# Kernel tuning notes

Measured on AMD Instinct MI355X. Metric: run time of the kernel, lower is better.

## Reference

```python
import jax, jax.numpy as jnp
import numpy as np

B, T, F, K = 32, 1500, 512, 31
QBITS = 8
EPS = 1e-5


def fake_quant(x, bits=QBITS):
    """Symmetric per-tensor fake quantization (scale from dynamic max-abs),
    with straight-through estimator so gradients pass through unchanged."""
    qmax = 2.0 ** (bits - 1) - 1.0  # 127 for 8 bits
    scale = jnp.maximum(jnp.max(jnp.abs(x)) / qmax, 1e-8)
    q = jnp.clip(jnp.round(x / scale), -qmax - 1.0, qmax) * scale
    return x + jax.lax.stop_gradient(q - x)


def setup_inputs() -> dict:
    key = jax.random.key(0)
    ks = jax.random.split(key, 5)
    x = jax.random.normal(ks[0], (B, T, F), dtype=jnp.float32)
    W1 = jax.random.normal(ks[1], (2 * F, F), dtype=jnp.float32) * (1.0 / np.sqrt(F))
    b1 = jnp.zeros((2 * F,), jnp.float32)
    dw_w = jax.random.normal(ks[2], (F, 1, K), dtype=jnp.float32) * (1.0 / np.sqrt(K))
    dw_b = jnp.zeros((F,), jnp.float32)
    W2 = jax.random.normal(ks[3], (F, F), dtype=jnp.float32) * (1.0 / np.sqrt(F))
    b2 = jnp.zeros((F,), jnp.float32)
    return {
        "x": x,
        "ln_gamma": jnp.ones((F,), jnp.float32),
        "ln_beta": jnp.zeros((F,), jnp.float32),
        "W1": W1, "b1": b1,
        "dw_w": dw_w, "dw_b": dw_b,
        "bn_gamma": jnp.ones((F,), jnp.float32),
        "bn_beta": jnp.zeros((F,), jnp.float32),
        "W2": W2, "b2": b2,
    }


def _forward(x, ln_gamma, ln_beta, W1, b1, dw_w, dw_b, bn_gamma, bn_beta, W2, b2):
    # LayerNorm over last dim F
    mu = jnp.mean(x, axis=-1, keepdims=True)
    var = jnp.mean(jnp.square(x - mu), axis=-1, keepdims=True)
    t = (x - mu) * jax.lax.rsqrt(var + EPS) * ln_gamma + ln_beta

    # pconv1 in-quant -> quantized pointwise conv1 (Linear F -> 2F) -> out-quant
    t = fake_quant(t)
    t = jnp.einsum("btf,gf->btg", t, fake_quant(W1)) + b1
    t = fake_quant(t)

    # GLU over last dim: [B,T,2F] -> [B,T,F]
    a, g = jnp.split(t, 2, axis=-1)
    t = a * jax.nn.sigmoid(g)

    # depthwise conv on [B,F,T]
    t = jnp.transpose(t, (0, 2, 1))  # [B,F,T]
    t = fake_quant(t)
    t = jax.lax.conv_general_dilated(
        t, fake_quant(dw_w),
        window_strides=(1,),
        padding=[((K - 1) // 2, (K - 1) // 2)],
        feature_group_count=F,
        dimension_numbers=("NCH", "OIH", "NCH"),
    ) + dw_b[None, :, None]
    t = fake_quant(t)

    # BatchNorm1d over channel dim (stats over batch and time), training-style batch stats
    bmu = jnp.mean(t, axis=(0, 2), keepdims=True)
    bvar = jnp.mean(jnp.square(t - bmu), axis=(0, 2), keepdims=True)
    t = (t - bmu) * jax.lax.rsqrt(bvar + EPS) * bn_gamma[None, :, None] + bn_beta[None, :, None]

    t = jnp.transpose(t, (0, 2, 1))  # [B,T,F]
    t = jax.nn.silu(t)

    # pconv2 in-quant -> quantized pointwise conv2 (Linear F -> F) -> out-quant
    t = fake_quant(t)
    t = jnp.einsum("btf,gf->btg", t, fake_quant(W2)) + b2
    t = fake_quant(t)
    return t  # dropout is identity (p=0 / eval)


def reference(x, ln_gamma, ln_beta, W1, b1, dw_w, dw_b, bn_gamma, bn_beta, W2, b2):
    return _forward(x, ln_gamma, ln_beta, W1, b1, dw_w, dw_b, bn_gamma, bn_beta, W2, b2)
```

## Files before the change

kernel.cpp:

```cpp
#include <hip/hip_runtime.h>
#include <stdint.h>

typedef __bf16 bf16;
typedef __bf16   bf16x4 __attribute__((ext_vector_type(4)));
typedef __bf16   bf16x8 __attribute__((ext_vector_type(8)));
typedef short    s16x8  __attribute__((ext_vector_type(8)));
typedef float    fx4    __attribute__((ext_vector_type(4)));

#define NB 32
#define NT 1500
#define NF 512
#define NM (NB*NT)
#define KW 31
#define EPSF 1e-5f

__device__ __forceinline__ float dscale(const float* a) {
  return fmaxf(a[0] * (1.0f/127.0f), 1e-8f);
}
__device__ __forceinline__ float fq_int(float x, float inv_s) {
  return fminf(fmaxf(rintf(x*inv_s), -128.0f), 127.0f);
}
__device__ __forceinline__ void block_amax(float v, float* dst) {
  __shared__ float red[8];
  #pragma unroll
  for (int o = 32; o > 0; o >>= 1) v = fmaxf(v, __shfl_xor(v, o));
  if ((threadIdx.x & 63) == 0) red[threadIdx.x >> 6] = v;
  __syncthreads();
  if (threadIdx.x == 0) {
    int nw = blockDim.x >> 6;
    float m = red[0];
    for (int i = 1; i < nw; i++) m = fmaxf(m, red[i]);
    atomicMax((unsigned int*)dst, __float_as_uint(m));
  }
}

__device__ __forceinline__ float amax_loop(const float* p, long n4, int bid, int gsz) {
  float am = 0.f;
  long i = (long)bid * blockDim.x + threadIdx.x;
  long stride = (long)gsz * blockDim.x;
  for (; i < n4; i += stride) {
    fx4 v = ((const fx4*)p)[i];
    #pragma unroll
    for (int j = 0; j < 4; j++) am = fmaxf(am, fabsf(v[j]));
  }
  return am;
}
__global__ void absmax_w(const float* __restrict__ W1, const float* __restrict__ W2,
                         const float* __restrict__ dwp, float* a) {
  int bx = blockIdx.x;
  float am; float* dst;
  if (bx < 256)      { am = amax_loop(W1,  131072, bx,       256); dst = a + 1; }
  else if (bx < 384) { am = amax_loop(W2,  65536,  bx - 256, 128); dst = a + 2; }
  else               { am = amax_loop(dwp, 3968,   bx - 384, 8);   dst = a + 3; }
  block_amax(am, dst);
}

__global__ void quant_pack(const float* __restrict__ src, bf16* __restrict__ dst,
                           int R, const float* amax) {
  float inv_s = 1.0f / dscale(amax);
  int total = R * 64;
  for (int t = blockIdx.x*blockDim.x + threadIdx.x; t < total; t += gridDim.x*blockDim.x) {
    int r = t >> 6, q8 = t & 63;
    const float* s = src + (size_t)r*512 + q8*8;
    fx4 v0 = *(const fx4*)s, v1 = *(const fx4*)(s+4);
    bf16x8 o;
    #pragma unroll
    for (int j = 0; j < 4; j++) { o[j] = (bf16)fq_int(v0[j], inv_s); o[4+j] = (bf16)fq_int(v1[j], inv_s); }
    int r16 = r >> 4, m16 = r & 15, kb = q8 >> 2, quad = q8 & 3;
    size_t chunk = ((size_t)r16*16 + kb)*64 + quad*16 + m16;
    ((bf16x8*)dst)[chunk] = o;
  }
}

__global__ void quant_deq_f32(float* __restrict__ p, long n4, const float* amax) {
  float s = dscale(amax);
  float inv_s = 1.0f / s;
  long i = (long)blockIdx.x * blockDim.x + threadIdx.x;
  long stride = (long)gridDim.x * blockDim.x;
  for (; i < n4; i += stride) {
    fx4 v = ((fx4*)p)[i];
    fx4 o;
    #pragma unroll
    for (int j = 0; j < 4; j++) o[j] = fq_int(v[j], inv_s) * s;
    ((fx4*)p)[i] = o;
  }
}

__global__ void ln_k(const float* __restrict__ x, const float* __restrict__ g,
                     const float* __restrict__ be, float* __restrict__ t, float* amax) {
  int lane = threadIdx.x & 63;
  int wavesTotal = (gridDim.x * blockDim.x) >> 6;
  int wave = ((blockIdx.x * blockDim.x) + threadIdx.x) >> 6;
  fx4 g0 = ((const fx4*)g)[lane],  g1 = ((const fx4*)g)[lane+64];
  fx4 b0 = ((const fx4*)be)[lane], b1v = ((const fx4*)be)[lane+64];
  float gf[8], bff[8];
  #pragma unroll
  for (int j = 0; j < 4; j++) { gf[j] = g0[j]; gf[4+j] = g1[j]; bff[j] = b0[j]; bff[4+j] = b1v[j]; }
  float am = 0.f;
  for (int row = wave; row < NM; row += wavesTotal) {
    const fx4* xr = (const fx4*)(x + (long)row*NF);
    fx4 x0 = xr[lane], x1 = xr[lane+64];
    float xf[8]; float s = 0.f;
    #pragma unroll
    for (int j = 0; j < 4; j++) { xf[j] = x0[j]; xf[4+j] = x1[j]; }
    #pragma unroll
    for (int j = 0; j < 8; j++) s += xf[j];
    #pragma unroll
    for (int o = 32; o > 0; o >>= 1) s += __shfl_xor(s, o);
    float mu = s * (1.0f/NF);
    float vs = 0.f;
    #pragma unroll
    for (int j = 0; j < 8; j++) { float d = xf[j]-mu; vs += d*d; }
    #pragma unroll
    for (int o = 32; o > 0; o >>= 1) vs += __shfl_xor(vs, o);
    float inv = rsqrtf(vs*(1.0f/NF) + EPSF);
    fx4 o0, o1;
    #pragma unroll
    for (int j = 0; j < 4; j++) {
      float v = (xf[j]-mu)*inv*gf[j] + bff[j];
      am = fmaxf(am, fabsf(v)); o0[j] = v;
    }
    #pragma unroll
    for (int j = 0; j < 4; j++) {
      float v = (xf[4+j]-mu)*inv*gf[4+j] + bff[4+j];
      am = fmaxf(am, fabsf(v)); o1[j] = v;
    }
    ((fx4*)(t + (long)row*NF))[lane]    = o0;
    ((fx4*)(t + (long)row*NF))[lane+64] = o1;
  }
  block_amax(am, amax);
}

template<int NBN, int MODE>
__global__ __launch_bounds__(256) void gemm_k(
    const bf16* __restrict__ A, const bf16* __restrict__ Bt,
    const float* __restrict__ bias, float* __restrict__ C,
    const float* amaxA, const float* amaxB, float* amaxC) {
  const int N = NBN * 128;
  int id = blockIdx.x;
  int bn = (id >> 3) % NBN;
  int bm = 8 * (id / (8 * NBN)) + (id & 7);
  if (bm >= 375) return;
  int lane = threadIdx.x & 63;
  int w = threadIdx.x >> 6;
  int wm = w >> 1, wn = w & 1;
  int quad = lane >> 4;
  int m16 = lane & 15;

  fx4 acc[4][4];
  #pragma unroll
  for (int i = 0; i < 4; i++)
    #pragma unroll
    for (int j = 0; j < 4; j++) acc[i][j] = fx4{0.f,0.f,0.f,0.f};

  const bf16* pA[4];
  const bf16* pB[4];
  #pragma unroll
  for (int i = 0; i < 4; i++)
    pA[i] = A + ((size_t)(bm*8 + wm*4 + i)*16)*512 + lane*8;
  #pragma unroll
  for (int j = 0; j < 4; j++)
    pB[j] = Bt + ((size_t)(bn*8 + wn*4 + j)*16)*512 + lane*8;

  #pragma unroll
  for (int kb = 0; kb < 16; kb++) {
    s16x8 aF[4], bF[4];
    #pragma unroll
    for (int i = 0; i < 4; i++) aF[i] = *(const s16x8*)(pA[i] + kb*512);
    #pragma unroll
    for (int j = 0; j < 4; j++) bF[j] = *(const s16x8*)(pB[j] + kb*512);
    #pragma unroll
    for (int i = 0; i < 4; i++)
      #pragma unroll
      for (int j = 0; j < 4; j++) {
        if (MODE == 0)
          acc[i][j] = __builtin_amdgcn_mfma_f32_16x16x32_bf16(aF[i], bF[j], acc[i][j], 0, 0, 0);
        else
          acc[i][j] = __builtin_amdgcn_mfma_f32_16x16x32_bf16(bF[j], aF[i], acc[i][j], 0, 0, 0);
      }
  }

  float ab = dscale(amaxA) * dscale(amaxB);
  float am = 0.f;
  if (MODE == 0) {
    #pragma unroll
    for (int j = 0; j < 4; j++) {
      int col = bn*128 + wn*64 + j*16 + m16;
      float bv = bias[col];
      #pragma unroll
      for (int i = 0; i < 4; i++) {
        int row0 = bm*128 + wm*64 + i*16 + quad*4;
        fx4 o;
        #pragma unroll
        for (int rr = 0; rr < 4; rr++) {
          float v = acc[i][j][rr]*ab + bv;
          am = fmaxf(am, fabsf(v)); o[rr] = v;
        }
        *(fx4*)(C + (size_t)col*NM + row0) = o;
      }
    }
  } else {
    #pragma unroll
    for (int i = 0; i < 4; i++) {
      int m = bm*128 + wm*64 + i*16 + m16;
      #pragma unroll
      for (int j = 0; j < 4; j++) {
        int n0 = bn*128 + wn*64 + j*16 + quad*4;
        fx4 bv = *(const fx4*)(bias + n0);
        fx4 o;
        #pragma unroll
        for (int rr = 0; rr < 4; rr++) {
          float v = acc[i][j][rr]*ab + bv[rr];
          am = fmaxf(am, fabsf(v)); o[rr] = v;
        }
        *(fx4*)(C + (size_t)m*N + n0) = o;
      }
    }
  }
  block_amax(am, amaxC);
}

__global__ void glu_k(const float* __restrict__ uT, float* __restrict__ v,
                      const float* amaxU, float* amaxV) {
  float s = dscale(amaxU);
  float inv_s = 1.0f / s;
  float am = 0.f;
  const int tid = threadIdx.x;
  const int npairs = (NB*NF)/2;
  for (int pr = blockIdx.x; pr < npairs; pr += gridDim.x) {
    int row0 = pr*2;
    for (int i = tid; i < 750; i += 256) {
      int r2 = (i >= 375) ? 1 : 0;
      int c = i - 375*r2;
      int row = row0 + r2;
      int b = row >> 9, f = row & (NF-1);
      long bt = (long)b*NT + c*4;
      fx4 a = *(const fx4*)(uT + (long)f*NM + bt);
      fx4 g = *(const fx4*)(uT + (long)(f+NF)*NM + bt);
      fx4 o;
      #pragma unroll
      for (int j = 0; j < 4; j++) {
        float av = fq_int(a[j], inv_s) * s;
        float gv = fq_int(g[j], inv_s) * s;
        float val = av * (1.0f/(1.0f + expf(-gv)));
        am = fmaxf(am, fabsf(val));
        o[j] = val;
      }
      *(fx4*)(v + (long)row*NT + c*4) = o;
    }
  }
  block_amax(am, amaxV);
}

__global__ void dwconv_k(const float* __restrict__ v, const float* __restrict__ w,
                         const float* __restrict__ wb, float* __restrict__ y,
                         const float* amaxV, const float* amaxW, float* amaxY) {
  __shared__ float z[2][1568];
  __shared__ float wl[2][32];
  float sv = dscale(amaxV); float inv_sv = 1.0f/sv;
  float sw = dscale(amaxW); float inv_sw = 1.0f/sw;
  float am = 0.f;
  const int tid = threadIdx.x;
  const int rr = tid >> 7;
  const int cl = tid & 127;
  const int npairs = (NB*NF)/2;
  for (int pr = blockIdx.x; pr < npairs; pr += gridDim.x) {
    int row0 = pr*2;
    __syncthreads();
    if (tid < 64) {
      int r2 = tid >> 5, k = tid & 31;
      if (k < KW) {
        int f = (row0 + r2) & (NF-1);
        wl[r2][k] = fq_int(w[f*KW + k], inv_sw) * sw;
      }
    }
    if (tid < 128) {
      int r2 = tid >> 6, jj = tid & 63;
      if (jj < 16) z[r2][jj] = 0.f;
      else         z[r2][1500 + jj] = 0.f;
    }
    const fx4* vp = (const fx4*)(v + (long)row0 * NT);
    for (int i = tid; i < 750; i += 256) {
      fx4 q = vp[i];
      int r2 = (i >= 375) ? 1 : 0;
      int ii = i - 375*r2;
      fx4 o;
      #pragma unroll
      for (int j = 0; j < 4; j++) o[j] = fq_int(q[j], inv_sv) * sv;
      *(fx4*)&z[r2][16 + 4*ii] = o;
    }
    __syncthreads();
    float wr[KW];
    #pragma unroll
    for (int k = 0; k < KW; k++) wr[k] = wl[rr][k];
    float bias = wb[(row0 + rr) & (NF-1)];
    long base = (long)(row0 + rr) * NT;
    #pragma unroll
    for (int pass = 0; pass < 3; pass++) {
      int c = cl + pass*128;
      if (c < 375) {
        int t0 = c*4;
        fx4 win[9];
        #pragma unroll
        for (int i = 0; i < 9; i++) win[i] = *(const fx4*)&z[rr][t0 + 4*i];
        float acc0 = bias, acc1 = bias, acc2 = bias, acc3 = bias;
        #pragma unroll
        for (int k = 0; k < KW; k++) {
          float wk = wr[k];
          acc0 += win[(k+1)>>2][(k+1)&3] * wk;
          acc1 += win[(k+2)>>2][(k+2)&3] * wk;
          acc2 += win[(k+3)>>2][(k+3)&3] * wk;
          acc3 += win[(k+4)>>2][(k+4)&3] * wk;
        }
        fx4 o = {acc0, acc1, acc2, acc3};
        #pragma unroll
        for (int j = 0; j < 4; j++) am = fmaxf(am, fabsf(o[j]));
        *(fx4*)&y[base + t0] = o;
      }
    }
  }
  block_amax(am, amaxY);
}

__global__ void bnstats_k(const float* __restrict__ y, const float* amaxY,
                          float* bn_mean, float* bn_rinv) {
  float sy = dscale(amaxY); float inv_sy = 1.0f/sy;
  int f = blockIdx.x;
  int s1 = 0, s2 = 0;
  for (int b = 0; b < NB; b++) {
    const fx4* base = (const fx4*)(y + ((long)b*NF + f)*NT);
    for (int i = threadIdx.x; i < NT/4; i += blockDim.x) {
      fx4 v = base[i];
      #pragma unroll
      for (int j = 0; j < 4; j++) {
        int q = (int)fq_int(v[j], inv_sy);
        s1 += q; s2 += q*q;
      }
    }
  }
  #pragma unroll
  for (int o = 32; o > 0; o >>= 1) { s1 += __shfl_xor(s1, o); s2 += __shfl_xor(s2, o); }
  __shared__ int rs1[4], rs2[4];
  if ((threadIdx.x & 63) == 0) { rs1[threadIdx.x>>6] = s1; rs2[threadIdx.x>>6] = s2; }
  __syncthreads();
  if (threadIdx.x == 0) {
    long long S1 = (long long)rs1[0]+rs1[1]+rs1[2]+rs1[3];
    long long S2 = (long long)rs2[0]+rs2[1]+rs2[2]+rs2[3];
    double s = (double)sy;
    double mean = (double)S1 * s / (double)NM;
    double var  = (double)S2 * s * s / (double)NM - mean*mean;
    bn_mean[f] = (float)mean;
    bn_rinv[f] = rsqrtf((float)var + EPSF);
  }
}

__global__ void bnsilu_k(const float* __restrict__ y, const float* __restrict__ bg,
                         const float* __restrict__ bb, const float* amaxY,
                         const float* bn_mean, const float* bn_rinv,
                         float* __restrict__ p, float* amaxP) {
  __shared__ float lds[32][33];
  float sy = dscale(amaxY); float inv_sy = 1.0f/sy;
  float am = 0.f;
  int tx = threadIdx.x & 31, ty = threadIdx.x >> 5;
  const int TTILES = (NT + 31)/32;
  const int ntile = NB * (NF/32) * TTILES;
  for (int tile = blockIdx.x; tile < ntile; tile += gridDim.x) {
    int b = tile / ((NF/32)*TTILES);
    int rem = tile % ((NF/32)*TTILES);
    int fT = rem / TTILES, tT = rem % TTILES;
    int f0 = fT*32, t0 = tT*32;
    __syncthreads();
    #pragma unroll
    for (int sI = 0; sI < 4; sI++) {
      int f = f0 + ty + sI*8;
      int t = t0 + tx;
      if (t < NT) {
        float zq = fq_int(y[((long)b*NF + f)*NT + t], inv_sy) * sy;
        float val = (zq - bn_mean[f])*bn_rinv[f]*bg[f] + bb[f];
        val = val / (1.0f + expf(-val));
        am = fmaxf(am, fabsf(val));
        lds[tx][ty + sI*8] = val;
      }
    }
    __syncthreads();
    #pragma unroll
    for (int sI = 0; sI < 4; sI++) {
      int t = t0 + ty + sI*8;
      if (t < NT)
        p[((long)b*NT + t)*NF + f0 + tx] = lds[ty + sI*8][tx];
    }
  }
  block_amax(am, amaxP);
}

extern "C" void kernel_launch(void* const* d_in, const int* in_sizes, int n_in,
                              void* d_out, int out_size, void* d_ws, size_t ws_size,
                              hipStream_t stream) {
  const float* x  = (const float*)d_in[0];
  const float* lg = (const float*)d_in[1];
  const float* lb = (const float*)d_in[2];
  const float* W1 = (const float*)d_in[3];
  const float* b1 = (const float*)d_in[4];
  const float* dw = (const float*)d_in[5];
  const float* db = (const float*)d_in[6];
  const float* bg = (const float*)d_in[7];
  const float* bb = (const float*)d_in[8];
  const float* W2 = (const float*)d_in[9];
  const float* b2 = (const float*)d_in[10];
  float* out = (float*)d_out;

  char* ws = (char*)d_ws;
  float* amax    = (float*)ws;
  float* bn_mean = (float*)(ws + 1024);
  float* bn_rinv = (float*)(ws + 4096);
  char* H = ws + 8192;
  float* t_raw = (float*)H;
  float* uT    = (float*)H;
  bf16*  t_q   = (bf16*)(H + 196608000);
  float* y     = (float*)H;
  float* p_raw = (float*)(H + 98304000);
  bf16*  p_q   = (bf16*)(H + 196608000);
  bf16*  W1q   = (bf16*)(H + 245760000);
  bf16*  W2q   = (bf16*)(H + 246808576);
  float* v = (float*)d_out;
  float* r = (float*)d_out;

  hipMemsetAsync(ws, 0, 8192, stream);

  absmax_w<<<392, 256, 0, stream>>>(W1, W2, dw, amax);
  quant_pack<<<256, 256, 0, stream>>>(W1, W1q, 1024, amax+1);
  quant_pack<<<128, 256, 0, stream>>>(W2, W2q, 512,  amax+2);

  ln_k<<<1536, 256, 0, stream>>>(x, lg, lb, t_raw, amax+0);
  quant_pack<<<4096, 256, 0, stream>>>(t_raw, t_q, NM, amax+0);
  gemm_k<8,0><<<3008, 256, 0, stream>>>(t_q, W1q, b1, uT, amax+0, amax+1, amax+4);
  glu_k<<<4096, 256, 0, stream>>>(uT, v, amax+4, amax+5);
  dwconv_k<<<2048, 256, 0, stream>>>(v, dw, db, y, amax+5, amax+3, amax+6);
  bnstats_k<<<512, 256, 0, stream>>>(y, amax+6, bn_mean, bn_rinv);
  bnsilu_k<<<4096, 256, 0, stream>>>(y, bg, bb, amax+6, bn_mean, bn_rinv, p_raw, amax+7);
  quant_pack<<<4096, 256, 0, stream>>>(p_raw, p_q, NM, amax+7);
  gemm_k<4,1><<<1504, 256, 0, stream>>>(p_q, W2q, b2, r, amax+7, amax+2, amax+8);
  quant_deq_f32<<<2048, 256, 0, stream>>>(out, 24576000/4, amax+8);
}
```

Baseline: 677.1 us.

## Stage GEMM operand panels through LDS via direct global-to-LDS loads

The GEMM kernel used to read A and B fragments straight from global memory into registers, so each wave fetched its own copies. It now cooperatively loads the block's A and B panels into a 32KB shared buffer with global_load_lds, in 8 K-steps. Each wave then reads its MFMA fragments from LDS, so operands are shared across the 2x2 wave grid and global traffic drops. The cost is two barriers per K-step with no double buffering, which serializes loads and compute and uses more LDS, which may reduce occupancy.

New measurement: 826.3 us. 22.0% more time.

```diff
diff --git a/kernel.cpp b/kernel.cpp
--- a/kernel.cpp
+++ b/kernel.cpp
@@ -147,37 +147,57 @@
   int quad = lane >> 4;
   int m16 = lane & 15;
 
+  __shared__ __align__(16) char lds[32768];
+
   fx4 acc[4][4];
   #pragma unroll
   for (int i = 0; i < 4; i++)
     #pragma unroll
     for (int j = 0; j < 4; j++) acc[i][j] = fx4{0.f,0.f,0.f,0.f};
 
-  const bf16* pA[4];
-  const bf16* pB[4];
-  #pragma unroll
-  for (int i = 0; i < 4; i++)
-    pA[i] = A + ((size_t)(bm*8 + wm*4 + i)*16)*512 + lane*8;
-  #pragma unroll
-  for (int j = 0; j < 4; j++)
-    pB[j] = Bt + ((size_t)(bn*8 + wn*4 + j)*16)*512 + lane*8;
-
-  #pragma unroll
-  for (int kb = 0; kb < 16; kb++) {
-    s16x8 aF[4], bF[4];
-    #pragma unroll
-    for (int i = 0; i < 4; i++) aF[i] = *(const s16x8*)(pA[i] + kb*512);
-    #pragma unroll
-    for (int j = 0; j < 4; j++) bF[j] = *(const s16x8*)(pB[j] + kb*512);
-    #pragma unroll
-    for (int i = 0; i < 4; i++)
-      #pragma unroll
-      for (int j = 0; j < 4; j++) {
-        if (MODE == 0)
-          acc[i][j] = __builtin_amdgcn_mfma_f32_16x16x32_bf16(aF[i], bF[j], acc[i][j], 0, 0, 0);
-        else
-          acc[i][j] = __builtin_amdgcn_mfma_f32_16x16x32_bf16(bF[j], aF[i], acc[i][j], 0, 0, 0);
-      }
+  const bf16* gpan[8];
+  #pragma unroll
+  for (int q = 0; q < 8; q++) {
+    int pp = w*8 + q;
+    int loc = pp & 15;
+    int r16 = loc >> 1;
+    const bf16* base = (pp < 16)
+        ? A  + ((size_t)(bm*8 + r16)*16) * 512
+        : Bt + ((size_t)(bn*8 + r16)*16) * 512;
+    gpan[q] = base + (size_t)(loc & 1) * 512 + lane * 8;
+  }
+
+  #pragma unroll
+  for (int s = 0; s < 8; s++) {
+    if (s) __syncthreads();
+    #pragma unroll
+    for (int q = 0; q < 8; q++) {
+      int pp = w*8 + q;
+      __builtin_amdgcn_global_load_lds(
+          (const __attribute__((address_space(1))) void*)(gpan[q] + (size_t)s*1024),
+          (__attribute__((address_space(3))) void*)&lds[pp*1024 + lane*16],
+          16, 0, 0);
+    }
+    __syncthreads();
+    #pragma unroll
+    for (int kbl = 0; kbl < 2; kbl++) {
+      s16x8 aF[4], bF[4];
+      #pragma unroll
+      for (int i = 0; i < 4; i++)
+        aF[i] = *(const s16x8*)&lds[((wm*4 + i)*2 + kbl)*1024 + lane*16];
+      #pragma unroll
+      for (int j = 0; j < 4; j++)
+        bF[j] = *(const s16x8*)&lds[(16 + (wn*4 + j)*2 + kbl)*1024 + lane*16];
+      #pragma unroll
+      for (int i = 0; i < 4; i++)
+        #pragma unroll
+        for (int j = 0; j < 4; j++) {
+          if (MODE == 0)
+            acc[i][j] = __builtin_amdgcn_mfma_f32_16x16x32_bf16(aF[i], bF[j], acc[i][j], 0, 0, 0);
+          else
+            acc[i][j] = __builtin_amdgcn_mfma_f32_16x16x32_bf16(bF[j], aF[i], acc[i][j], 0, 0, 0);
+        }
+    }
   }
 
   float ab = dscale(amaxA) * dscale(amaxB);
```

## Recompute LayerNorm and derive SiLU absmax analytically to skip fp32 intermediates

Applied to the files above, without the earlier changes.

LayerNorm now runs twice over x: once to get the absmax and once to normalize, quantize and pack straight to bf16 in the GEMM tile layout. This removes the fp32 t_raw write and its re-read by quant_pack. For the BN+SiLU stage, bnstats computes the absmax of the post-SiLU values from the range of quantized integer levels per channel, since each channel maps to at most 256 distinct values. That lets bnsilu write packed bf16 directly and drops the p_raw buffer and one quant_pack pass. The cost is an extra full read of x and somewhat more work in bnstats.

Result: faster. 620.9 us (-8.3%).

```diff
diff --git a/kernel.cpp b/kernel.cpp
--- a/kernel.cpp
+++ b/kernel.cpp
@@ -86,20 +86,20 @@
   }
 }
 
-__global__ void ln_k(const float* __restrict__ x, const float* __restrict__ g,
-                     const float* __restrict__ be, float* __restrict__ t, float* amax) {
+__global__ void ln_amax_k(const float* __restrict__ x, const float* __restrict__ g,
+                          const float* __restrict__ be, float* amax) {
   int lane = threadIdx.x & 63;
   int wavesTotal = (gridDim.x * blockDim.x) >> 6;
   int wave = ((blockIdx.x * blockDim.x) + threadIdx.x) >> 6;
-  fx4 g0 = ((const fx4*)g)[lane],  g1 = ((const fx4*)g)[lane+64];
-  fx4 b0 = ((const fx4*)be)[lane], b1v = ((const fx4*)be)[lane+64];
+  fx4 g0 = ((const fx4*)g)[2*lane],  g1 = ((const fx4*)g)[2*lane+1];
+  fx4 b0 = ((const fx4*)be)[2*lane], b1v = ((const fx4*)be)[2*lane+1];
   float gf[8], bff[8];
   #pragma unroll
   for (int j = 0; j < 4; j++) { gf[j] = g0[j]; gf[4+j] = g1[j]; bff[j] = b0[j]; bff[4+j] = b1v[j]; }
   float am = 0.f;
   for (int row = wave; row < NM; row += wavesTotal) {
     const fx4* xr = (const fx4*)(x + (long)row*NF);
-    fx4 x0 = xr[lane], x1 = xr[lane+64];
+    fx4 x0 = xr[2*lane], x1 = xr[2*lane+1];
     float xf[8]; float s = 0.f;
     #pragma unroll
     for (int j = 0; j < 4; j++) { xf[j] = x0[j]; xf[4+j] = x1[j]; }
@@ -114,21 +114,54 @@
     #pragma unroll
     for (int o = 32; o > 0; o >>= 1) vs += __shfl_xor(vs, o);
     float inv = rsqrtf(vs*(1.0f/NF) + EPSF);
-    fx4 o0, o1;
-    #pragma unroll
-    for (int j = 0; j < 4; j++) {
+    #pragma unroll
+    for (int j = 0; j < 8; j++) {
       float v = (xf[j]-mu)*inv*gf[j] + bff[j];
-      am = fmaxf(am, fabsf(v)); o0[j] = v;
-    }
-    #pragma unroll
-    for (int j = 0; j < 4; j++) {
-      float v = (xf[4+j]-mu)*inv*gf[4+j] + bff[4+j];
-      am = fmaxf(am, fabsf(v)); o1[j] = v;
-    }
-    ((fx4*)(t + (long)row*NF))[lane]    = o0;
-    ((fx4*)(t + (long)row*NF))[lane+64] = o1;
+      am = fmaxf(am, fabsf(v));
+    }
   }
   block_amax(am, amax);
+}
+
+__global__ void ln_pack_k(const float* __restrict__ x, const float* __restrict__ g,
+                          const float* __restrict__ be, bf16* __restrict__ dst,
+                          const float* amax) {
+  int lane = threadIdx.x & 63;
+  int wavesTotal = (gridDim.x * blockDim.x) >> 6;
+  int wave = ((blockIdx.x * blockDim.x) + threadIdx.x) >> 6;
+  float inv_s = 1.0f / dscale(amax);
+  fx4 g0 = ((const fx4*)g)[2*lane],  g1 = ((const fx4*)g)[2*lane+1];
+  fx4 b0 = ((const fx4*)be)[2*lane], b1v = ((const fx4*)be)[2*lane+1];
+  float gf[8], bff[8];
+  #pragma unroll
+  for (int j = 0; j < 4; j++) { gf[j] = g0[j]; gf[4+j] = g1[j]; bff[j] = b0[j]; bff[4+j] = b1v[j]; }
+  for (int row = wave; row < NM; row += wavesTotal) {
+    const fx4* xr = (const fx4*)(x + (long)row*NF);
+    fx4 x0 = xr[2*lane], x1 = xr[2*lane+1];
+    float xf[8]; float s = 0.f;
+    #pragma unroll
+    for (int j = 0; j < 4; j++) { xf[j] = x0[j]; xf[4+j] = x1[j]; }
+    #pragma unroll
+    for (int j = 0; j < 8; j++) s += xf[j];
+    #pragma unroll
+    for (int o = 32; o > 0; o >>= 1) s += __shfl_xor(s, o);
+    float mu = s * (1.0f/NF);
+    float vs = 0.f;
+    #pragma unroll
+    for (int j = 0; j < 8; j++) { float d = xf[j]-mu; vs += d*d; }
+    #pragma unroll
+    for (int o = 32; o > 0; o >>= 1) vs += __shfl_xor(vs, o);
+    float inv = rsqrtf(vs*(1.0f/NF) + EPSF);
+    bf16x8 o8;
+    #pragma unroll
+    for (int j = 0; j < 8; j++) {
+      float v = (xf[j]-mu)*inv*gf[j] + bff[j];
+      o8[j] = (bf16)fq_int(v, inv_s);
+    }
+    int r16 = row >> 4, m16 = row & 15;
+    size_t chunk = ((size_t)r16*16 + (lane>>2))*64 + (lane&3)*16 + m16;
+    ((bf16x8*)dst)[chunk] = o8;
+  }
 }
 
 template<int NBN, int MODE>
@@ -323,10 +356,11 @@
 }
 
 __global__ void bnstats_k(const float* __restrict__ y, const float* amaxY,
-                          float* bn_mean, float* bn_rinv) {
+                          const float* __restrict__ bg, const float* __restrict__ bb,
+                          float* bn_mean, float* bn_rinv, float* amaxP) {
   float sy = dscale(amaxY); float inv_sy = 1.0f/sy;
   int f = blockIdx.x;
-  int s1 = 0, s2 = 0;
+  int s1 = 0, s2 = 0, qmn = 127, qmx = -128;
   for (int b = 0; b < NB; b++) {
     const fx4* base = (const fx4*)(y + ((long)b*NF + f)*NT);
     for (int i = threadIdx.x; i < NT/4; i += blockDim.x) {
@@ -335,13 +369,21 @@
       for (int j = 0; j < 4; j++) {
         int q = (int)fq_int(v[j], inv_sy);
         s1 += q; s2 += q*q;
-      }
-    }
-  }
-  #pragma unroll
-  for (int o = 32; o > 0; o >>= 1) { s1 += __shfl_xor(s1, o); s2 += __shfl_xor(s2, o); }
-  __shared__ int rs1[4], rs2[4];
-  if ((threadIdx.x & 63) == 0) { rs1[threadIdx.x>>6] = s1; rs2[threadIdx.x>>6] = s2; }
+        qmn = min(qmn, q); qmx = max(qmx, q);
+      }
+    }
+  }
+  #pragma unroll
+  for (int o = 32; o > 0; o >>= 1) {
+    s1 += __shfl_xor(s1, o); s2 += __shfl_xor(s2, o);
+    qmn = min(qmn, __shfl_xor(qmn, o)); qmx = max(qmx, __shfl_xor(qmx, o));
+  }
+  __shared__ int rs1[4], rs2[4], rmn[4], rmx[4];
+  __shared__ float sh_mean, sh_rinv; __shared__ int sh_qmn, sh_qmx;
+  if ((threadIdx.x & 63) == 0) {
+    int wv = threadIdx.x >> 6;
+    rs1[wv] = s1; rs2[wv] = s2; rmn[wv] = qmn; rmx[wv] = qmx;
+  }
   __syncthreads();
   if (threadIdx.x == 0) {
     long long S1 = (long long)rs1[0]+rs1[1]+rs1[2]+rs1[3];
@@ -349,18 +391,32 @@
     double s = (double)sy;
     double mean = (double)S1 * s / (double)NM;
     double var  = (double)S2 * s * s / (double)NM - mean*mean;
-    bn_mean[f] = (float)mean;
-    bn_rinv[f] = rsqrtf((float)var + EPSF);
-  }
-}
-
-__global__ void bnsilu_k(const float* __restrict__ y, const float* __restrict__ bg,
-                         const float* __restrict__ bb, const float* amaxY,
-                         const float* bn_mean, const float* bn_rinv,
-                         float* __restrict__ p, float* amaxP) {
+    float fm = (float)mean;
+    float fr = rsqrtf((float)var + EPSF);
+    bn_mean[f] = fm; bn_rinv[f] = fr;
+    sh_mean = fm; sh_rinv = fr;
+    sh_qmn = min(min(rmn[0],rmn[1]), min(rmn[2],rmn[3]));
+    sh_qmx = max(max(rmx[0],rmx[1]), max(rmx[2],rmx[3]));
+  }
+  __syncthreads();
+  float pm = 0.f;
+  int q = sh_qmn + (int)threadIdx.x;
+  if (q <= sh_qmx) {
+    float zq = (float)q * sy;
+    float val = (zq - sh_mean)*sh_rinv*bg[f] + bb[f];
+    val = val / (1.0f + expf(-val));
+    pm = fabsf(val);
+  }
+  block_amax(pm, amaxP);
+}
+
+__global__ void bnsilu_pack_k(const float* __restrict__ y, const float* __restrict__ bg,
+                              const float* __restrict__ bb, const float* amaxY,
+                              const float* bn_mean, const float* bn_rinv,
+                              bf16* __restrict__ pq, const float* amaxP) {
   __shared__ float lds[32][33];
   float sy = dscale(amaxY); float inv_sy = 1.0f/sy;
-  float am = 0.f;
+  float inv_sp = 1.0f / dscale(amaxP);
   int tx = threadIdx.x & 31, ty = threadIdx.x >> 5;
   const int TTILES = (NT + 31)/32;
   const int ntile = NB * (NF/32) * TTILES;
@@ -378,19 +434,25 @@
         float zq = fq_int(y[((long)b*NF + f)*NT + t], inv_sy) * sy;
         float val = (zq - bn_mean[f])*bn_rinv[f]*bg[f] + bb[f];
         val = val / (1.0f + expf(-val));
-        am = fmaxf(am, fabsf(val));
         lds[tx][ty + sI*8] = val;
       }
     }
     __syncthreads();
-    #pragma unroll
-    for (int sI = 0; sI < 4; sI++) {
-      int t = t0 + ty + sI*8;
-      if (t < NT)
-        p[((long)b*NT + t)*NF + f0 + tx] = lds[ty + sI*8][tx];
-    }
-  }
-  block_amax(am, amaxP);
+    if (threadIdx.x < 128) {
+      int r = threadIdx.x >> 2;
+      int c = threadIdx.x & 3;
+      int t = t0 + r;
+      if (t < NT) {
+        bf16x8 o8;
+        #pragma unroll
+        for (int j = 0; j < 8; j++) o8[j] = (bf16)fq_int(lds[r][c*8 + j], inv_sp);
+        long bt = (long)b*NT + t;
+        int q8 = (f0 >> 3) + c;
+        size_t chunk = ((size_t)(bt>>4)*16 + (q8>>2))*64 + (q8&3)*16 + (bt&15);
+        ((bf16x8*)pq)[chunk] = o8;
+      }
+    }
+  }
 }
 
 extern "C" void kernel_launch(void* const* d_in, const int* in_sizes, int n_in,
@@ -414,11 +476,9 @@
   float* bn_mean = (float*)(ws + 1024);
   float* bn_rinv = (float*)(ws + 4096);
   char* H = ws + 8192;
-  float* t_raw = (float*)H;
   float* uT    = (float*)H;
   bf16*  t_q   = (bf16*)(H + 196608000);
   float* y     = (float*)H;
-  float* p_raw = (float*)(H + 98304000);
   bf16*  p_q   = (bf16*)(H + 196608000);
   bf16*  W1q   = (bf16*)(H + 245760000);
   bf16*  W2q   = (bf16*)(H + 246808576);
@@ -431,14 +491,13 @@
   quant_pack<<<256, 256, 0, stream>>>(W1, W1q, 1024, amax+1);
   quant_pack<<<128, 256, 0, stream>>>(W2, W2q, 512,  amax+2);
 
-  ln_k<<<1536, 256, 0, stream>>>(x, lg, lb, t_raw, amax+0);
-  quant_pack<<<4096, 256, 0, stream>>>(t_raw, t_q, NM, amax+0);
+  ln_amax_k<<<1536, 256, 0, stream>>>(x, lg, lb, amax+0);
+  ln_pack_k<<<3072, 256, 0, stream>>>(x, lg, lb, t_q, amax+0);
   gemm_k<8,0><<<3008, 256, 0, stream>>>(t_q, W1q, b1, uT, amax+0, amax+1, amax+4);
   glu_k<<<4096, 256, 0, stream>>>(uT, v, amax+4, amax+5);
   dwconv_k<<<2048, 256, 0, stream>>>(v, dw, db, y, amax+5, amax+3, amax+6);
-  bnstats_k<<<512, 256, 0, stream>>>(y, amax+6, bn_mean, bn_rinv);
-  bnsilu_k<<<4096, 256, 0, stream>>>(y, bg, bb, amax+6, bn_mean, bn_rinv, p_raw, amax+7);
-  quant_pack<<<4096, 256, 0, stream>>>(p_raw, p_q, NM, amax+7);
+  bnstats_k<<<512, 256, 0, stream>>>(y, amax+6, bg, bb, bn_mean, bn_rinv, amax+7);
+  bnsilu_pack_k<<<4096, 256, 0, stream>>>(y, bg, bb, amax+6, bn_mean, bn_rinv, p_q, amax+7);
   gemm_k<4,1><<<1504, 256, 0, stream>>>(p_q, W2q, b2, r, amax+7, amax+2, amax+8);
   quant_deq_f32<<<2048, 256, 0, stream>>>(out, 24576000/4, amax+8);
 }
```
